# Optimization experiments

Measured on AMD Instinct MI355X. Metric: run time of the kernel, lower is better.

## Reference

```python
import jax, jax.numpy as jnp
import numpy as np

N_NODES = 50000
N_EDGES = 800000
IN_DIM = 128
EDGE_DIM = 16
HIDDEN = 128
N_LAYERS = 3
N_GRAPHS = 256
BN_EPS = 1e-5


def setup_inputs() -> dict:
    key = jax.random.key(0)
    ks = jax.random.split(key, 24)
    s = 0.05
    inp = {
        "x": jax.random.normal(ks[0], (N_NODES, IN_DIM), jnp.float32),
        "edge_index": jax.random.randint(ks[1], (2, N_EDGES), 0, N_NODES, jnp.int32),
        "edge_attr": jax.random.normal(ks[2], (N_EDGES, EDGE_DIM), jnp.float32),
        "batch": jnp.sort(jax.random.randint(ks[3], (N_NODES,), 0, N_GRAPHS, jnp.int32)),
        "n_graphs": N_GRAPHS,
        # input projection
        "lin_in_w": jax.random.normal(ks[4], (IN_DIM, HIDDEN), jnp.float32) * s,
        "lin_in_b": jnp.zeros((HIDDEN,), jnp.float32),
        # per-layer message MLP (stacked over layers)
        "msg_w1": jax.random.normal(ks[5], (N_LAYERS, HIDDEN + EDGE_DIM, HIDDEN), jnp.float32) * s,
        "msg_b1": jnp.zeros((N_LAYERS, HIDDEN), jnp.float32),
        "msg_w2": jax.random.normal(ks[6], (N_LAYERS, HIDDEN, HIDDEN), jnp.float32) * s,
        "msg_b2": jnp.zeros((N_LAYERS, HIDDEN), jnp.float32),
        # BatchNorm (eval mode: running stats)
        "bn_gamma": jnp.ones((N_LAYERS, HIDDEN), jnp.float32),
        "bn_beta": jnp.zeros((N_LAYERS, HIDDEN), jnp.float32),
        "bn_mean": jax.random.normal(ks[7], (N_LAYERS, HIDDEN), jnp.float32) * 0.01,
        "bn_var": jax.random.uniform(ks[8], (N_LAYERS, HIDDEN), jnp.float32, 0.5, 1.5),
        # GRUCell params (PyTorch layout: [3*H, H], gate order r,z,n)
        "gru_wih": jax.random.normal(ks[9], (N_LAYERS, 3 * HIDDEN, HIDDEN), jnp.float32) * s,
        "gru_whh": jax.random.normal(ks[10], (N_LAYERS, 3 * HIDDEN, HIDDEN), jnp.float32) * s,
        "gru_bih": jnp.zeros((N_LAYERS, 3 * HIDDEN), jnp.float32),
        "gru_bhh": jnp.zeros((N_LAYERS, 3 * HIDDEN), jnp.float32),
        # readout linear: [2H -> H]
        "ro_w": jax.random.normal(ks[11], (2 * HIDDEN, HIDDEN), jnp.float32) * s,
        "ro_b": jnp.zeros((HIDDEN,), jnp.float32),
    }
    return inp


def _gru_cell(x, h, wih, whh, bih, bhh):
    gi = x @ wih.T + bih  # [N, 3H]
    gh = h @ whh.T + bhh
    ir, iz, inn = jnp.split(gi, 3, axis=1)
    hr, hz, hn = jnp.split(gh, 3, axis=1)
    r = jax.nn.sigmoid(ir + hr)
    z = jax.nn.sigmoid(iz + hz)
    n = jnp.tanh(inn + r * hn)
    return (1.0 - z) * n + z * h


def reference(x, edge_index, edge_attr, batch, n_graphs,
              lin_in_w, lin_in_b, msg_w1, msg_b1, msg_w2, msg_b2,
              bn_gamma, bn_beta, bn_mean, bn_var,
              gru_wih, gru_whh, gru_bih, gru_bhh, ro_w, ro_b):
    h = jax.nn.relu(x @ lin_in_w + lin_in_b)  # [N, H]
    src, dst = edge_index[0], edge_index[1]
    n_nodes = h.shape[0]
    for l in range(N_LAYERS):
        m_in = jnp.concatenate([h[src], edge_attr], axis=1)  # [E, H+Ed]
        m = jax.nn.relu(m_in @ msg_w1[l] + msg_b1[l]) @ msg_w2[l] + msg_b2[l]  # [E, H]
        agg = jax.ops.segment_sum(m, dst, num_segments=n_nodes)  # scatter-add
        h_new = _gru_cell(agg, h, gru_wih[l], gru_whh[l], gru_bih[l], gru_bhh[l])
        bn = (h_new - bn_mean[l]) * jax.lax.rsqrt(bn_var[l] + BN_EPS) * bn_gamma[l] + bn_beta[l]
        h = h + bn  # dropout is identity in eval mode
    # readout: segment mean + segment max over graphs
    cnt = jax.ops.segment_sum(jnp.ones((n_nodes, 1), h.dtype), batch, num_segments=n_graphs)
    z_sum = jax.ops.segment_sum(h, batch, num_segments=n_graphs)
    z_mean = z_sum / jnp.maximum(cnt, 1.0)
    z_max = jax.ops.segment_max(h, batch, num_segments=n_graphs)
    z_max = jnp.where(cnt > 0, z_max, 0.0)  # empty graphs -> 0 (as in torch code)
    z = jax.nn.relu(jnp.concatenate([z_mean, z_max], axis=1) @ ro_w + ro_b)
    return z
```

## Files before the change

### kernel.cpp

```cpp
#include <hip/hip_runtime.h>
#include <math.h>

constexpr int NN = 50000;
constexpr int NE = 800000;
constexpr int H  = 128;
constexpr int ED = 16;
constexpr int NL = 3;
constexpr int NG = 256;
constexpr int NBINS = 50176;
constexpr int TE = 128;

typedef __attribute__((ext_vector_type(8))) short bf8;
typedef __attribute__((ext_vector_type(4))) float f32x4;

__device__ __forceinline__ unsigned short f2bf(float f) {
    unsigned u = __float_as_uint(f);
    unsigned r = (u + 0x7FFFu + ((u >> 16) & 1u)) >> 16;
    return (unsigned short)r;
}
__device__ __forceinline__ float bf2f(unsigned short b) {
    return __uint_as_float(((unsigned)b) << 16);
}
__device__ __forceinline__ float fsig(float x) {
    float e = __expf(fminf(-x, 80.f));
    return 1.f / (1.f + e);
}
__device__ __forceinline__ float ftanh_(float x) {
    float e = __expf(fminf(-2.f * x, 80.f));
    return (1.f - e) / (1.f + e);
}

__global__ __launch_bounds__(256) void k_sort_zero(int* __restrict__ counts) {
    int i = blockIdx.x * 256 + threadIdx.x;
    counts[i] = 0;
}

__global__ __launch_bounds__(256) void k_hist(const int* __restrict__ ei,
                                              int* __restrict__ counts) {
    int e = blockIdx.x * 256 + threadIdx.x;
    if (e < NE) atomicAdd(&counts[ei[NE + e]], 1);
}

__global__ __launch_bounds__(256) void k_scan1(const int* __restrict__ counts,
                                               int* __restrict__ incl,
                                               int* __restrict__ bsum) {
    __shared__ int s[256];
    int t = threadIdx.x;
    int i = blockIdx.x * 256 + t;
    int v = counts[i];
    s[t] = v;
    __syncthreads();
    #pragma unroll
    for (int off = 1; off < 256; off <<= 1) {
        int x = (t >= off) ? s[t - off] : 0;
        __syncthreads();
        s[t] += x;
        __syncthreads();
    }
    incl[i] = s[t];
    if (t == 255) bsum[blockIdx.x] = s[255];
}

__global__ __launch_bounds__(256) void k_scan2(int* __restrict__ bsum) {
    __shared__ int s[256];
    int t = threadIdx.x;
    int v = (t < 196) ? bsum[t] : 0;
    s[t] = v;
    __syncthreads();
    #pragma unroll
    for (int off = 1; off < 256; off <<= 1) {
        int x = (t >= off) ? s[t - off] : 0;
        __syncthreads();
        s[t] += x;
        __syncthreads();
    }
    if (t < 196) bsum[t] = s[t] - v;
}

__global__ __launch_bounds__(256) void k_scan3(const int* __restrict__ counts,
                                               const int* __restrict__ incl,
                                               const int* __restrict__ bsum,
                                               int* __restrict__ cur) {
    int i = blockIdx.x * 256 + threadIdx.x;
    cur[i] = incl[i] - counts[i] + bsum[blockIdx.x];
}

__global__ __launch_bounds__(256) void k_scatter_perm(const int* __restrict__ ei,
                                                      int* __restrict__ cur,
                                                      int* __restrict__ perm) {
    int e = blockIdx.x * 256 + threadIdx.x;
    if (e < NE) {
        int d = ei[NE + e];
        int pos = atomicAdd(&cur[d], 1);
        perm[pos] = e;
    }
}

__global__ __launch_bounds__(256) void k_gather(const int* __restrict__ ei,
                                                const float* __restrict__ ea,
                                                int* __restrict__ perm,
                                                int* __restrict__ dsts,
                                                unsigned short* __restrict__ ea_bf) {
    int i = blockIdx.x * 256 + threadIdx.x;
    if (i >= NE) return;
    int e = perm[i];
    perm[i] = ei[e];
    dsts[i] = ei[NE + e];
    const float4* sp = (const float4*)(ea + (size_t)e * ED);
    float4 v0 = sp[0], v1 = sp[1], v2 = sp[2], v3 = sp[3];
    union { uint4 u[2]; unsigned short sh[16]; } pk;
    pk.sh[0] = f2bf(v0.x); pk.sh[1] = f2bf(v0.y); pk.sh[2] = f2bf(v0.z); pk.sh[3] = f2bf(v0.w);
    pk.sh[4] = f2bf(v1.x); pk.sh[5] = f2bf(v1.y); pk.sh[6] = f2bf(v1.z); pk.sh[7] = f2bf(v1.w);
    pk.sh[8] = f2bf(v2.x); pk.sh[9] = f2bf(v2.y); pk.sh[10] = f2bf(v2.z); pk.sh[11] = f2bf(v2.w);
    pk.sh[12] = f2bf(v3.x); pk.sh[13] = f2bf(v3.y); pk.sh[14] = f2bf(v3.z); pk.sh[15] = f2bf(v3.w);
    uint4* d4 = (uint4*)(ea_bf + (size_t)i * 16);
    d4[0] = pk.u[0];
    d4[1] = pk.u[1];
}

__global__ __launch_bounds__(256) void k_prep(const float* __restrict__ wih,
                                              const float* __restrict__ whh,
                                              const float* __restrict__ w1,
                                              const float* __restrict__ w2,
                                              const float* __restrict__ lin_w,
                                              unsigned short* __restrict__ wgru,
                                              unsigned short* __restrict__ w1et,
                                              unsigned short* __restrict__ w2t,
                                              unsigned short* __restrict__ w1ht,
                                              unsigned short* __restrict__ winT) {
    int i = blockIdx.x * 256 + threadIdx.x;
    if (i < 294912) {
        int m = i / 147456, rem = i % 147456;
        wgru[i] = f2bf((m == 0 ? wih : whh)[rem]);
        return;
    }
    i -= 294912;
    if (i < NL * 128 * 32) {
        int l = i / 4096, rem = i % 4096;
        int n = rem >> 5, k = rem & 31;
        float v = (k < ED) ? w1[(size_t)l * 144 * 128 + (size_t)(128 + k) * 128 + n] : 0.f;
        w1et[i] = f2bf(v);
        return;
    }
    i -= NL * 128 * 32;
    if (i < NL * 128 * 128) {
        int l = i / 16384, rem = i % 16384;
        int n = rem >> 7, k = rem & 127;
        w2t[i] = f2bf(w2[(size_t)l * 16384 + (size_t)k * 128 + n]);
        return;
    }
    i -= NL * 128 * 128;
    if (i < NL * 128 * 128) {
        int l = i / 16384, rem = i % 16384;
        int n = rem >> 7, k = rem & 127;
        w1ht[i] = f2bf(w1[(size_t)l * 144 * 128 + (size_t)k * 128 + n]);
        return;
    }
    i -= NL * 128 * 128;
    if (i < 128 * 128) {
        int n = i >> 7, k = i & 127;
        winT[i] = f2bf(lin_w[k * 128 + n]);
    }
}

__global__ __launch_bounds__(256) void k_inproj(const float* __restrict__ x,
                                                const unsigned short* __restrict__ winT,
                                                const float* __restrict__ bias,
                                                const unsigned short* __restrict__ w1h0,
                                                float* __restrict__ h,
                                                unsigned short* __restrict__ p_bf,
                                                float* __restrict__ agg) {
    __shared__ unsigned short As[32][136];
    const int t = threadIdx.x;
    const int w = t >> 6, lane = t & 63, l15 = lane & 15, q = lane >> 4;
    const int n0 = blockIdx.x * 32;

    bf8 bfr[2][4];
    #pragma unroll
    for (int nt = 0; nt < 2; ++nt) {
        int n = w * 32 + nt * 16 + l15;
        #pragma unroll
        for (int ks = 0; ks < 4; ++ks)
            bfr[nt][ks] = *(const bf8*)(winT + (size_t)n * 128 + ks * 32 + q * 8);
    }

    {
        int r = t >> 3, cs = (t & 7) * 16;
        int row = n0 + r;
        float4 v[4];
        if (row < NN) {
            const float4* src = (const float4*)(x + (size_t)row * H + cs);
            #pragma unroll
            for (int j = 0; j < 4; ++j) v[j] = src[j];
        } else {
            #pragma unroll
            for (int j = 0; j < 4; ++j) v[j] = make_float4(0.f, 0.f, 0.f, 0.f);
        }
        union { uint4 u[2]; unsigned short s[16]; } pk;
        #pragma unroll
        for (int j = 0; j < 4; ++j) {
            pk.s[j * 4 + 0] = f2bf(v[j].x); pk.s[j * 4 + 1] = f2bf(v[j].y);
            pk.s[j * 4 + 2] = f2bf(v[j].z); pk.s[j * 4 + 3] = f2bf(v[j].w);
        }
        *(uint4*)&As[r][cs] = pk.u[0];
        *(uint4*)&As[r][cs + 8] = pk.u[1];
    }
    __syncthreads();

    {
        int r = t >> 3, cs = (t & 7) * 16;
        int row = n0 + r;
        if (row < NN) {
            float4 z = make_float4(0.f, 0.f, 0.f, 0.f);
            float4* dz = (float4*)(agg + (size_t)row * H + cs);
            dz[0] = z; dz[1] = z; dz[2] = z; dz[3] = z;
        }
    }

    f32x4 acc[2][2];
    #pragma unroll
    for (int mt = 0; mt < 2; ++mt)
        #pragma unroll
        for (int nt = 0; nt < 2; ++nt) acc[mt][nt] = {0.f, 0.f, 0.f, 0.f};

    #pragma unroll
    for (int ks = 0; ks < 4; ++ks) {
        #pragma unroll
        for (int mt = 0; mt < 2; ++mt) {
            bf8 af = *(const bf8*)&As[mt * 16 + l15][ks * 32 + q * 8];
            acc[mt][0] = __builtin_amdgcn_mfma_f32_16x16x32_bf16(af, bfr[0][ks], acc[mt][0], 0, 0, 0);
            acc[mt][1] = __builtin_amdgcn_mfma_f32_16x16x32_bf16(af, bfr[1][ks], acc[mt][1], 0, 0, 0);
        }
    }
    __syncthreads();

    #pragma unroll
    for (int nt = 0; nt < 2; ++nt) {
        int col = w * 32 + nt * 16 + l15;
        float bv = bias[col];
        #pragma unroll
        for (int mt = 0; mt < 2; ++mt) {
            #pragma unroll
            for (int r = 0; r < 4; ++r) {
                int nl = mt * 16 + q * 4 + r;
                int node = n0 + nl;
                float v = fmaxf(acc[mt][nt][r] + bv, 0.f);
                if (node < NN) h[(size_t)node * H + col] = v;
                As[nl][col] = f2bf(v);
            }
        }
    }
    __syncthreads();

    bf8 pfr[2][4];
    #pragma unroll
    for (int nt = 0; nt < 2; ++nt) {
        int n = w * 32 + nt * 16 + l15;
        #pragma unroll
        for (int ks = 0; ks < 4; ++ks)
            pfr[nt][ks] = *(const bf8*)(w1h0 + (size_t)n * 128 + ks * 32 + q * 8);
    }
    f32x4 accp[2][2];
    #pragma unroll
    for (int mt = 0; mt < 2; ++mt)
        #pragma unroll
        for (int nt = 0; nt < 2; ++nt) accp[mt][nt] = {0.f, 0.f, 0.f, 0.f};
    #pragma unroll
    for (int ks = 0; ks < 4; ++ks) {
        #pragma unroll
        for (int mt = 0; mt < 2; ++mt) {
            bf8 af = *(const bf8*)&As[mt * 16 + l15][ks * 32 + q * 8];
            accp[mt][0] = __builtin_amdgcn_mfma_f32_16x16x32_bf16(af, pfr[0][ks], accp[mt][0], 0, 0, 0);
            accp[mt][1] = __builtin_amdgcn_mfma_f32_16x16x32_bf16(af, pfr[1][ks], accp[mt][1], 0, 0, 0);
        }
    }
    #pragma unroll
    for (int nt = 0; nt < 2; ++nt) {
        int col = w * 32 + nt * 16 + l15;
        #pragma unroll
        for (int mt = 0; mt < 2; ++mt) {
            #pragma unroll
            for (int r = 0; r < 4; ++r) {
                int node = n0 + mt * 16 + q * 4 + r;
                if (node < NN) p_bf[(size_t)node * H + col] = f2bf(accp[mt][nt][r]);
            }
        }
    }
}

__global__ __launch_bounds__(256, 4) void k_edge_mfma(
        const unsigned short* __restrict__ p,
        const int* __restrict__ srcs,
        const int* __restrict__ dsts,
        const unsigned short* __restrict__ ea_bf,
        const unsigned short* __restrict__ w1et,
        const float* __restrict__ b1,
        const unsigned short* __restrict__ w2t,
        const float* __restrict__ b2,
        float* __restrict__ agg) {
    __shared__ unsigned short u_s[TE][136];
    __shared__ int src_s[TE], dst_s[TE];

    const int t    = threadIdx.x;
    const int w    = t >> 6;
    const int lane = t & 63;
    const int l15  = lane & 15;
    const int q    = lane >> 4;

    bf8 w1f[2];
    bf8 w2f[2][4];
    float b1v[2], b2v[2];
    #pragma unroll
    for (int nt = 0; nt < 2; ++nt) {
        int n = w * 32 + nt * 16 + l15;
        w1f[nt] = *(const bf8*)(w1et + (size_t)n * 32 + q * 8);
        #pragma unroll
        for (int ks = 0; ks < 4; ++ks)
            w2f[nt][ks] = *(const bf8*)(w2t + (size_t)n * 128 + ks * 32 + q * 8);
        b1v[nt] = b1[n];
        b2v[nt] = b2[n];
    }

    const f32x4 zero = {0.f, 0.f, 0.f, 0.f};

    for (int base = blockIdx.x * TE; base < NE; base += gridDim.x * TE) {
        if (t < TE) src_s[t] = srcs[base + t];
        else        dst_s[t - TE] = dsts[base + t - TE];
        __syncthreads();

        {
            int row = t >> 4, seg = t & 15;
            #pragma unroll
            for (int it = 0; it < 8; ++it) {
                int rr = row + 16 * it;
                *(uint4*)&u_s[rr][seg * 8] =
                    *(const uint4*)(p + (size_t)src_s[rr] * H + seg * 8);
            }
        }

        #pragma unroll
        for (int half = 0; half < 2; ++half) {
            f32x4 acc1[4][2];
            #pragma unroll
            for (int m4 = 0; m4 < 4; ++m4) {
                int mt = half * 4 + m4;
                bf8 af = {0, 0, 0, 0, 0, 0, 0, 0};
                if (q < 2)
                    af = *(const bf8*)(ea_bf + (size_t)(base + mt * 16 + l15) * 16 + q * 8);
                acc1[m4][0] = __builtin_amdgcn_mfma_f32_16x16x32_bf16(af, w1f[0], zero, 0, 0, 0);
                acc1[m4][1] = __builtin_amdgcn_mfma_f32_16x16x32_bf16(af, w1f[1], zero, 0, 0, 0);
            }
            if (half == 0) __syncthreads();
            #pragma unroll
            for (int m4 = 0; m4 < 4; ++m4) {
                #pragma unroll
                for (int r = 0; r < 4; ++r) {
                    int er = (half * 4 + m4) * 16 + q * 4 + r;
                    #pragma unroll
                    for (int nt = 0; nt < 2; ++nt) {
                        int col = w * 32 + nt * 16 + l15;
                        float v = acc1[m4][nt][r] + bf2f(u_s[er][col]) + b1v[nt];
                        u_s[er][col] = f2bf(fmaxf(v, 0.f));
                    }
                }
            }
        }
        __syncthreads();

        #pragma unroll
        for (int half = 0; half < 2; ++half) {
            f32x4 acc2[4][2];
            #pragma unroll
            for (int m4 = 0; m4 < 4; ++m4)
                #pragma unroll
                for (int nt = 0; nt < 2; ++nt) acc2[m4][nt] = zero;
            #pragma unroll
            for (int ks = 0; ks < 4; ++ks) {
                #pragma unroll
                for (int m4 = 0; m4 < 4; ++m4) {
                    int mt = half * 4 + m4;
                    bf8 af = *(const bf8*)&u_s[mt * 16 + l15][ks * 32 + q * 8];
                    acc2[m4][0] = __builtin_amdgcn_mfma_f32_16x16x32_bf16(af, w2f[0][ks], acc2[m4][0], 0, 0, 0);
                    acc2[m4][1] = __builtin_amdgcn_mfma_f32_16x16x32_bf16(af, w2f[1][ks], acc2[m4][1], 0, 0, 0);
                }
            }
            __syncthreads();
            #pragma unroll
            for (int m4 = 0; m4 < 4; ++m4) {
                #pragma unroll
                for (int r = 0; r < 4; ++r) {
                    int er = (half * 4 + m4) * 16 + q * 4 + r;
                    #pragma unroll
                    for (int nt = 0; nt < 2; ++nt) {
                        int col = w * 32 + nt * 16 + l15;
                        u_s[er][col] = f2bf(acc2[m4][nt][r] + b2v[nt]);
                    }
                }
            }
        }
        __syncthreads();

        {
            int c = t & 127, hh = t >> 7;
            float* aggc = agg + c;
            float sum = 0.f;
            int prev = dst_s[hh * 64];
            #pragma unroll 4
            for (int i = 0; i < 64; ++i) {
                int e = hh * 64 + i;
                int d = dst_s[e];
                float v = bf2f(u_s[e][c]);
                if (d != prev) {
                    atomicAdd(aggc + (size_t)prev * H, sum);
                    sum = 0.f;
                    prev = d;
                }
                sum += v;
            }
            atomicAdd(aggc + (size_t)prev * H, sum);
        }
        __syncthreads();
    }
}

__global__ __launch_bounds__(256) void k_gru_mfma(float* __restrict__ agg,
                                                  float* __restrict__ h,
                                                  const unsigned short* __restrict__ wih,
                                                  const unsigned short* __restrict__ whh,
                                                  const float* __restrict__ bih,
                                                  const float* __restrict__ bhh,
                                                  const float* __restrict__ gamma,
                                                  const float* __restrict__ beta,
                                                  const float* __restrict__ mean,
                                                  const float* __restrict__ var,
                                                  const unsigned short* __restrict__ w1h_next,
                                                  unsigned short* __restrict__ p_bf,
                                                  int* __restrict__ ro_z) {
    __shared__ unsigned short ab[32][136];
    __shared__ unsigned short hb[32][136];
    __shared__ float hf[32][132];
    const int t = threadIdx.x;
    const int w = t >> 6, lane = t & 63, l15 = lane & 15, q = lane >> 4;
    const int n0 = blockIdx.x * 32;

    {
        int r = t >> 3, cs = (t & 7) * 16;
        int row = n0 + r;
        float4 va[4], vh[4];
        if (row < NN) {
            const float4* sa = (const float4*)(agg + (size_t)row * H + cs);
            const float4* sh = (const float4*)(h + (size_t)row * H + cs);
            #pragma unroll
            for (int j = 0; j < 4; ++j) { va[j] = sa[j]; vh[j] = sh[j]; }
        } else {
            #pragma unroll
            for (int j = 0; j < 4; ++j) {
                va[j] = make_float4(0.f, 0.f, 0.f, 0.f);
                vh[j] = va[j];
            }
        }
        union { uint4 u[2]; unsigned short s[16]; } pa, ph;
        #pragma unroll
        for (int j = 0; j < 4; ++j) {
            pa.s[j * 4 + 0] = f2bf(va[j].x); pa.s[j * 4 + 1] = f2bf(va[j].y);
            pa.s[j * 4 + 2] = f2bf(va[j].z); pa.s[j * 4 + 3] = f2bf(va[j].w);
            ph.s[j * 4 + 0] = f2bf(vh[j].x); ph.s[j * 4 + 1] = f2bf(vh[j].y);
            ph.s[j * 4 + 2] = f2bf(vh[j].z); ph.s[j * 4 + 3] = f2bf(vh[j].w);
            *(float4*)&hf[r][cs + j * 4] = vh[j];
        }
        *(uint4*)&ab[r][cs] = pa.u[0];  *(uint4*)&ab[r][cs + 8] = pa.u[1];
        *(uint4*)&hb[r][cs] = ph.u[0];  *(uint4*)&hb[r][cs + 8] = ph.u[1];
    }
    __syncthreads();

    if (w1h_next != nullptr) {
        int r = t >> 3, cs = (t & 7) * 16;
        int row = n0 + r;
        if (row < NN) {
            float4 z = make_float4(0.f, 0.f, 0.f, 0.f);
            float4* dz = (float4*)(agg + (size_t)row * H + cs);
            dz[0] = z; dz[1] = z; dz[2] = z; dz[3] = z;
        }
    }
    if (ro_z != nullptr && blockIdx.x < 257) ro_z[blockIdx.x * 256 + t] = 0;

    f32x4 acc[2][2][3][2];
    #pragma unroll
    for (int mt = 0; mt < 2; ++mt)
        #pragma unroll
        for (int io = 0; io < 2; ++io)
            #pragma unroll
            for (int g = 0; g < 3; ++g)
                #pragma unroll
                for (int nt = 0; nt < 2; ++nt) acc[mt][io][g][nt] = {0.f, 0.f, 0.f, 0.f};

    #pragma unroll
    for (int ks = 0; ks < 4; ++ks) {
        bf8 a_a[2], a_h[2];
        #pragma unroll
        for (int mt = 0; mt < 2; ++mt) {
            a_a[mt] = *(const bf8*)&ab[mt * 16 + l15][ks * 32 + q * 8];
            a_h[mt] = *(const bf8*)&hb[mt * 16 + l15][ks * 32 + q * 8];
        }
        #pragma unroll
        for (int g = 0; g < 3; ++g) {
            #pragma unroll
            for (int nt = 0; nt < 2; ++nt) {
                int n = g * 128 + w * 32 + nt * 16 + l15;
                bf8 bi = *(const bf8*)(wih + (size_t)n * 128 + ks * 32 + q * 8);
                bf8 bh = *(const bf8*)(whh + (size_t)n * 128 + ks * 32 + q * 8);
                #pragma unroll
                for (int mt = 0; mt < 2; ++mt) {
                    acc[mt][0][g][nt] = __builtin_amdgcn_mfma_f32_16x16x32_bf16(a_a[mt], bi, acc[mt][0][g][nt], 0, 0, 0);
                    acc[mt][1][g][nt] = __builtin_amdgcn_mfma_f32_16x16x32_bf16(a_h[mt], bh, acc[mt][1][g][nt], 0, 0, 0);
                }
            }
        }
    }

    float rout[2][2][4];
    #pragma unroll
    for (int nt = 0; nt < 2; ++nt) {
        int col = w * 32 + nt * 16 + l15;
        float bir = bih[col], biz = bih[128 + col], bin = bih[256 + col];
        float bhr = bhh[col], bhz = bhh[128 + col], bhn = bhh[256 + col];
        float ga = gamma[col], be = beta[col], mu = mean[col];
        float iv = rsqrtf(var[col] + 1e-5f);
        #pragma unroll
        for (int mt = 0; mt < 2; ++mt) {
            #pragma unroll
            for (int r = 0; r < 4; ++r) {
                int nl = mt * 16 + q * 4 + r;
                int node = n0 + nl;
                float ir = acc[mt][0][0][nt][r] + bir;
                float iz = acc[mt][0][1][nt][r] + biz;
                float in = acc[mt][0][2][nt][r] + bin;
                float hr = acc[mt][1][0][nt][r] + bhr;
                float hz = acc[mt][1][1][nt][r] + bhz;
                float hn = acc[mt][1][2][nt][r] + bhn;
                float rg = fsig(ir + hr);
                float zg = fsig(iz + hz);
                float ng = ftanh_(in + rg * hn);
                float hv = hf[nl][col];
                float hnew = (1.f - zg) * ng + zg * hv;
                float bn = (hnew - mu) * iv * ga + be;
                float out = hv + bn;
                rout[nt][mt][r] = out;
                if (node < NN) h[(size_t)node * H + col] = out;
            }
        }
    }

    if (w1h_next != nullptr) {
        __syncthreads();
        #pragma unroll
        for (int nt = 0; nt < 2; ++nt) {
            int col = w * 32 + nt * 16 + l15;
            #pragma unroll
            for (int mt = 0; mt < 2; ++mt)
                #pragma unroll
                for (int r = 0; r < 4; ++r)
                    hb[mt * 16 + q * 4 + r][col] = f2bf(rout[nt][mt][r]);
        }
        __syncthreads();

        f32x4 accp[2][2];
        #pragma unroll
        for (int mt = 0; mt < 2; ++mt)
            #pragma unroll
            for (int nt = 0; nt < 2; ++nt) accp[mt][nt] = {0.f, 0.f, 0.f, 0.f};
        #pragma unroll
        for (int ks = 0; ks < 4; ++ks) {
            bf8 pf0, pf1;
            {
                int n = w * 32 + l15;
                pf0 = *(const bf8*)(w1h_next + (size_t)n * 128 + ks * 32 + q * 8);
                pf1 = *(const bf8*)(w1h_next + (size_t)(n + 16) * 128 + ks * 32 + q * 8);
            }
            #pragma unroll
            for (int mt = 0; mt < 2; ++mt) {
                bf8 af = *(const bf8*)&hb[mt * 16 + l15][ks * 32 + q * 8];
                accp[mt][0] = __builtin_amdgcn_mfma_f32_16x16x32_bf16(af, pf0, accp[mt][0], 0, 0, 0);
                accp[mt][1] = __builtin_amdgcn_mfma_f32_16x16x32_bf16(af, pf1, accp[mt][1], 0, 0, 0);
            }
        }
        #pragma unroll
        for (int nt = 0; nt < 2; ++nt) {
            int col = w * 32 + nt * 16 + l15;
            #pragma unroll
            for (int mt = 0; mt < 2; ++mt) {
                #pragma unroll
                for (int r = 0; r < 4; ++r) {
                    int node = n0 + mt * 16 + q * 4 + r;
                    if (node < NN) p_bf[(size_t)node * H + col] = f2bf(accp[mt][nt][r]);
                }
            }
        }
    }
}

__device__ __forceinline__ unsigned fkey(float f) {
    unsigned b = __float_as_uint(f);
    return (b & 0x80000000u) ? ~b : (b | 0x80000000u);
}
__device__ __forceinline__ float funkey(unsigned k) {
    unsigned b = (k & 0x80000000u) ? (k & 0x7FFFFFFFu) : ~k;
    return __uint_as_float(b);
}

__global__ __launch_bounds__(256) void k_ro_scan(const float* __restrict__ h,
                                                 const int* __restrict__ batch,
                                                 float* __restrict__ gsum,
                                                 unsigned* __restrict__ gmaxb,
                                                 float* __restrict__ gcnt) {
    __shared__ int bt_s[64];
    const int t = threadIdx.x;
    const int n0 = blockIdx.x * 64;
    if (t < 64) bt_s[t] = (n0 + t < NN) ? batch[n0 + t] : -1;
    __syncthreads();

    int c = t & 127, hh = t >> 7;
    float sum = 0.f, mx = -3.4e38f, cnt = 0.f;
    int prev = bt_s[hh * 32];
    #pragma unroll 4
    for (int i = 0; i < 32; ++i) {
        int e = hh * 32 + i;
        int g = bt_s[e];
        if (g != prev) {
            if (prev >= 0) {
                atomicAdd(&gsum[prev * H + c], sum);
                atomicMax(&gmaxb[prev * H + c], fkey(mx));
                if (c == 0) atomicAdd(&gcnt[prev], cnt);
            }
            sum = 0.f; mx = -3.4e38f; cnt = 0.f;
            prev = g;
        }
        if (g >= 0) {
            float v = h[(size_t)(n0 + e) * H + c];
            sum += v;
            mx = fmaxf(mx, v);
            cnt += 1.f;
        }
    }
    if (prev >= 0) {
        atomicAdd(&gsum[prev * H + c], sum);
        atomicMax(&gmaxb[prev * H + c], fkey(mx));
        if (c == 0) atomicAdd(&gcnt[prev], cnt);
    }
}

__global__ __launch_bounds__(128) void k_ro_final(const float* __restrict__ gsum,
                                                  const unsigned* __restrict__ gmaxb,
                                                  const float* __restrict__ gcnt,
                                                  const float* __restrict__ row,
                                                  const float* __restrict__ rob,
                                                  float* __restrict__ out) {
    __shared__ float cat[256];
    const int g = blockIdx.x, t = threadIdx.x;
    float cnt = gcnt[g];
    float inv = 1.f / fmaxf(cnt, 1.f);
    cat[t] = gsum[g * H + t] * inv;
    float mx = funkey(gmaxb[g * H + t]);
    cat[128 + t] = (cnt > 0.f) ? mx : 0.f;
    __syncthreads();
    float acc = rob[t];
    #pragma unroll 4
    for (int k = 0; k < 256; ++k) acc += cat[k] * row[k * H + t];
    out[g * H + t] = fmaxf(acc, 0.f);
}

extern "C" void kernel_launch(void* const* d_in, const int* in_sizes, int n_in,
                              void* d_out, int out_size, void* d_ws, size_t ws_size,
                              hipStream_t stream) {
    const float* x        = (const float*)d_in[0];
    const int*   ei       = (const int*)d_in[1];
    const float* ea       = (const float*)d_in[2];
    const int*   batch    = (const int*)d_in[3];
    const float* lin_in_w = (const float*)d_in[5];
    const float* lin_in_b = (const float*)d_in[6];
    const float* msg_w1   = (const float*)d_in[7];
    const float* msg_b1   = (const float*)d_in[8];
    const float* msg_w2   = (const float*)d_in[9];
    const float* msg_b2   = (const float*)d_in[10];
    const float* bn_gamma = (const float*)d_in[11];
    const float* bn_beta  = (const float*)d_in[12];
    const float* bn_mean  = (const float*)d_in[13];
    const float* bn_var   = (const float*)d_in[14];
    const float* gru_wih  = (const float*)d_in[15];
    const float* gru_whh  = (const float*)d_in[16];
    const float* gru_bih  = (const float*)d_in[17];
    const float* gru_bhh  = (const float*)d_in[18];
    const float* ro_w     = (const float*)d_in[19];
    const float* ro_b     = (const float*)d_in[20];

    float* ws = (float*)d_ws;
    float*          h     = ws;
    float*          agg   = ws + 6400000;
    unsigned short* p_bf  = (unsigned short*)(ws + 12800000);
    float*          gsum  = ws + 16000000;
    unsigned*       gmaxb = (unsigned*)(ws + 16032768);
    float*          gcnt  = ws + 16065536;
    unsigned short* wgru  = (unsigned short*)(ws + 16065792);
    unsigned short* w1et  = (unsigned short*)(ws + 16213248);
    unsigned short* w2t   = (unsigned short*)(ws + 16219392);
    unsigned short* w1ht  = (unsigned short*)(ws + 16243968);
    unsigned short* winT  = (unsigned short*)(ws + 16268544);
    int*            cnts  = (int*)(ws + 16276736);
    int*            incl  = (int*)(ws + 16326912);
    int*            cur   = (int*)(ws + 16377088);
    int*            bsum  = (int*)(ws + 16427264);
    int*            srcs  = (int*)(ws + 16427520);
    int*            dsts  = (int*)(ws + 17227520);
    unsigned short* ea_bf = (unsigned short*)(ws + 18027520);

    k_prep<<<1648, 256, 0, stream>>>(gru_wih, gru_whh, msg_w1, msg_w2, lin_in_w,
                                     wgru, w1et, w2t, w1ht, winT);
    k_sort_zero<<<196, 256, 0, stream>>>(cnts);
    k_hist<<<3125, 256, 0, stream>>>(ei, cnts);
    k_scan1<<<196, 256, 0, stream>>>(cnts, incl, bsum);
    k_scan2<<<1, 256, 0, stream>>>(bsum);
    k_scan3<<<196, 256, 0, stream>>>(cnts, incl, bsum, cur);
    k_scatter_perm<<<3125, 256, 0, stream>>>(ei, cur, srcs);
    k_gather<<<3125, 256, 0, stream>>>(ei, ea, srcs, dsts, ea_bf);

    k_inproj<<<1563, 256, 0, stream>>>(x, winT, lin_in_b, w1ht, h, p_bf, agg);

    for (int l = 0; l < NL; ++l) {
        k_edge_mfma<<<1024, 256, 0, stream>>>(p_bf, srcs, dsts, ea_bf,
                                              w1et + (size_t)l * 4096, msg_b1 + l * 128,
                                              w2t + (size_t)l * 16384, msg_b2 + l * 128,
                                              agg);
        const unsigned short* w1h_next = (l + 1 < NL) ? (w1ht + (size_t)(l + 1) * 16384) : nullptr;
        int* ro_z = (l == NL - 1) ? (int*)gsum : nullptr;
        k_gru_mfma<<<1563, 256, 0, stream>>>(agg, h,
                                             wgru + (size_t)l * 49152,
                                             wgru + (size_t)(NL + l) * 49152,
                                             gru_bih + l * 384, gru_bhh + l * 384,
                                             bn_gamma + l * 128, bn_beta + l * 128,
                                             bn_mean + l * 128, bn_var + l * 128,
                                             w1h_next, p_bf, ro_z);
    }

    k_ro_scan<<<782, 256, 0, stream>>>(h, batch, gsum, gmaxb, gcnt);
    k_ro_final<<<NG, 128, 0, stream>>>(gsum, gmaxb, gcnt, ro_w, ro_b, (float*)d_out);
}
```

Before: 803.3 us.

## Merge preprocessing kernels, single-block scan, prefetch edge indices, pair scatter-add channels

Folds the count-zeroing into the weight prep kernel and replaces the three-kernel prefix scan with a single 1024-thread block, cutting several small launches. In the edge kernel, src/dst indices for the next tile are double-buffered in shared memory so one barrier per iteration can be dropped. The segmented scatter-add now has each thread handle two adjacent channels over 32 edges instead of one channel over 64. The single-block scan serializes work onto one CU, and correctness of the removed trailing barrier depends on the next iteration's barrier ordering.

```diff
diff --git a/kernel.cpp b/kernel.cpp
--- a/kernel.cpp
+++ b/kernel.cpp
@@ -9,6 +9,7 @@
 constexpr int NG = 256;
 constexpr int NBINS = 50176;
 constexpr int TE = 128;
+constexpr int PREP_TOTAL = 294912 + NL*128*32 + NL*128*128 + NL*128*128 + 128*128;
 
 typedef __attribute__((ext_vector_type(8))) short bf8;
 typedef __attribute__((ext_vector_type(4))) float f32x4;
@@ -30,9 +31,53 @@
     return (1.f - e) / (1.f + e);
 }
 
-__global__ __launch_bounds__(256) void k_sort_zero(int* __restrict__ counts) {
+__global__ __launch_bounds__(256) void k_prep(const float* __restrict__ wih,
+                                              const float* __restrict__ whh,
+                                              const float* __restrict__ w1,
+                                              const float* __restrict__ w2,
+                                              const float* __restrict__ lin_w,
+                                              unsigned short* __restrict__ wgru,
+                                              unsigned short* __restrict__ w1et,
+                                              unsigned short* __restrict__ w2t,
+                                              unsigned short* __restrict__ w1ht,
+                                              unsigned short* __restrict__ winT,
+                                              int* __restrict__ cnts) {
     int i = blockIdx.x * 256 + threadIdx.x;
-    counts[i] = 0;
+    if (i < 294912) {
+        int m = i / 147456, rem = i % 147456;
+        wgru[i] = f2bf((m == 0 ? wih : whh)[rem]);
+        return;
+    }
+    i -= 294912;
+    if (i < NL * 128 * 32) {
+        int l = i / 4096, rem = i % 4096;
+        int n = rem >> 5, k = rem & 31;
+        float v = (k < ED) ? w1[(size_t)l * 144 * 128 + (size_t)(128 + k) * 128 + n] : 0.f;
+        w1et[i] = f2bf(v);
+        return;
+    }
+    i -= NL * 128 * 32;
+    if (i < NL * 128 * 128) {
+        int l = i / 16384, rem = i % 16384;
+        int n = rem >> 7, k = rem & 127;
+        w2t[i] = f2bf(w2[(size_t)l * 16384 + (size_t)k * 128 + n]);
+        return;
+    }
+    i -= NL * 128 * 128;
+    if (i < NL * 128 * 128) {
+        int l = i / 16384, rem = i % 16384;
+        int n = rem >> 7, k = rem & 127;
+        w1ht[i] = f2bf(w1[(size_t)l * 144 * 128 + (size_t)k * 128 + n]);
+        return;
+    }
+    i -= NL * 128 * 128;
+    if (i < 128 * 128) {
+        int n = i >> 7, k = i & 127;
+        winT[i] = f2bf(lin_w[k * 128 + n]);
+        return;
+    }
+    i -= 128 * 128;
+    if (i < NBINS) cnts[i] = 0;
 }
 
 __global__ __launch_bounds__(256) void k_hist(const int* __restrict__ ei,
@@ -41,48 +86,30 @@
     if (e < NE) atomicAdd(&counts[ei[NE + e]], 1);
 }
 
-__global__ __launch_bounds__(256) void k_scan1(const int* __restrict__ counts,
-                                               int* __restrict__ incl,
-                                               int* __restrict__ bsum) {
-    __shared__ int s[256];
-    int t = threadIdx.x;
-    int i = blockIdx.x * 256 + t;
-    int v = counts[i];
-    s[t] = v;
+__global__ __launch_bounds__(1024) void k_scan_all(const int* __restrict__ cnts,
+                                                   int* __restrict__ cur) {
+    __shared__ int s[1024];
+    const int t = threadIdx.x;
+    const int b0 = t * 49;
+    int sum = 0;
+    #pragma unroll 7
+    for (int i = 0; i < 49; ++i) sum += cnts[b0 + i];
+    s[t] = sum;
     __syncthreads();
     #pragma unroll
-    for (int off = 1; off < 256; off <<= 1) {
+    for (int off = 1; off < 1024; off <<= 1) {
         int x = (t >= off) ? s[t - off] : 0;
         __syncthreads();
         s[t] += x;
         __syncthreads();
     }
-    incl[i] = s[t];
-    if (t == 255) bsum[blockIdx.x] = s[255];
-}
-
-__global__ __launch_bounds__(256) void k_scan2(int* __restrict__ bsum) {
-    __shared__ int s[256];
-    int t = threadIdx.x;
-    int v = (t < 196) ? bsum[t] : 0;
-    s[t] = v;
-    __syncthreads();
-    #pragma unroll
-    for (int off = 1; off < 256; off <<= 1) {
-        int x = (t >= off) ? s[t - off] : 0;
-        __syncthreads();
-        s[t] += x;
-        __syncthreads();
-    }
-    if (t < 196) bsum[t] = s[t] - v;
-}
-
-__global__ __launch_bounds__(256) void k_scan3(const int* __restrict__ counts,
-                                               const int* __restrict__ incl,
-                                               const int* __restrict__ bsum,
-                                               int* __restrict__ cur) {
-    int i = blockIdx.x * 256 + threadIdx.x;
-    cur[i] = incl[i] - counts[i] + bsum[blockIdx.x];
+    int run = s[t] - sum;
+    #pragma unroll 7
+    for (int i = 0; i < 49; ++i) {
+        int c = cnts[b0 + i];
+        cur[b0 + i] = run;
+        run += c;
+    }
 }
 
 __global__ __launch_bounds__(256) void k_scatter_perm(const int* __restrict__ ei,
@@ -118,51 +145,6 @@
     d4[1] = pk.u[1];
 }
 
-__global__ __launch_bounds__(256) void k_prep(const float* __restrict__ wih,
-                                              const float* __restrict__ whh,
-                                              const float* __restrict__ w1,
-                                              const float* __restrict__ w2,
-                                              const float* __restrict__ lin_w,
-                                              unsigned short* __restrict__ wgru,
-                                              unsigned short* __restrict__ w1et,
-                                              unsigned short* __restrict__ w2t,
-                                              unsigned short* __restrict__ w1ht,
-                                              unsigned short* __restrict__ winT) {
-    int i = blockIdx.x * 256 + threadIdx.x;
-    if (i < 294912) {
-        int m = i / 147456, rem = i % 147456;
-        wgru[i] = f2bf((m == 0 ? wih : whh)[rem]);
-        return;
-    }
-    i -= 294912;
-    if (i < NL * 128 * 32) {
-        int l = i / 4096, rem = i % 4096;
-        int n = rem >> 5, k = rem & 31;
-        float v = (k < ED) ? w1[(size_t)l * 144 * 128 + (size_t)(128 + k) * 128 + n] : 0.f;
-        w1et[i] = f2bf(v);
-        return;
-    }
-    i -= NL * 128 * 32;
-    if (i < NL * 128 * 128) {
-        int l = i / 16384, rem = i % 16384;
-        int n = rem >> 7, k = rem & 127;
-        w2t[i] = f2bf(w2[(size_t)l * 16384 + (size_t)k * 128 + n]);
-        return;
-    }
-    i -= NL * 128 * 128;
-    if (i < NL * 128 * 128) {
-        int l = i / 16384, rem = i % 16384;
-        int n = rem >> 7, k = rem & 127;
-        w1ht[i] = f2bf(w1[(size_t)l * 144 * 128 + (size_t)k * 128 + n]);
-        return;
-    }
-    i -= NL * 128 * 128;
-    if (i < 128 * 128) {
-        int n = i >> 7, k = i & 127;
-        winT[i] = f2bf(lin_w[k * 128 + n]);
-    }
-}
-
 __global__ __launch_bounds__(256) void k_inproj(const float* __restrict__ x,
                                                 const unsigned short* __restrict__ winT,
                                                 const float* __restrict__ bias,
@@ -299,7 +281,7 @@
         const float* __restrict__ b2,
         float* __restrict__ agg) {
     __shared__ unsigned short u_s[TE][136];
-    __shared__ int src_s[TE], dst_s[TE];
+    __shared__ int src_s[2][TE], dst_s[2][TE];
 
     const int t    = threadIdx.x;
     const int w    = t >> 6;
@@ -323,9 +305,16 @@
 
     const f32x4 zero = {0.f, 0.f, 0.f, 0.f};
 
+    {
+        int base0 = blockIdx.x * TE;
+        if (base0 < NE) {
+            if (t < TE) src_s[0][t] = srcs[base0 + t];
+            else        dst_s[0][t - TE] = dsts[base0 + t - TE];
+        }
+    }
+    int pb = 0;
+
     for (int base = blockIdx.x * TE; base < NE; base += gridDim.x * TE) {
-        if (t < TE) src_s[t] = srcs[base + t];
-        else        dst_s[t - TE] = dsts[base + t - TE];
         __syncthreads();
 
         {
@@ -334,7 +323,7 @@
             for (int it = 0; it < 8; ++it) {
                 int rr = row + 16 * it;
                 *(uint4*)&u_s[rr][seg * 8] =
-                    *(const uint4*)(p + (size_t)src_s[rr] * H + seg * 8);
+                    *(const uint4*)(p + (size_t)src_s[pb][rr] * H + seg * 8);
             }
         }
 
@@ -401,25 +390,37 @@
         __syncthreads();
 
         {
-            int c = t & 127, hh = t >> 7;
-            float* aggc = agg + c;
-            float sum = 0.f;
-            int prev = dst_s[hh * 64];
+            int nbase = base + gridDim.x * TE;
+            if (nbase < NE) {
+                if (t < TE) src_s[1 - pb][t] = srcs[nbase + t];
+                else        dst_s[1 - pb][t - TE] = dsts[nbase + t - TE];
+            }
+        }
+
+        {
+            int q4 = t >> 6;
+            int cp = t & 63;
+            float* aggc = agg + (cp << 1);
+            float s0 = 0.f, s1 = 0.f;
+            int prev = dst_s[pb][q4 * 32];
             #pragma unroll 4
-            for (int i = 0; i < 64; ++i) {
-                int e = hh * 64 + i;
-                int d = dst_s[e];
-                float v = bf2f(u_s[e][c]);
+            for (int i = 0; i < 32; ++i) {
+                int e = q4 * 32 + i;
+                int d = dst_s[pb][e];
+                unsigned v = *(const unsigned*)&u_s[e][cp << 1];
                 if (d != prev) {
-                    atomicAdd(aggc + (size_t)prev * H, sum);
-                    sum = 0.f;
+                    atomicAdd(aggc + (size_t)prev * H, s0);
+                    atomicAdd(aggc + (size_t)prev * H + 1, s1);
+                    s0 = 0.f; s1 = 0.f;
                     prev = d;
                 }
-                sum += v;
-            }
-            atomicAdd(aggc + (size_t)prev * H, sum);
-        }
-        __syncthreads();
+                s0 += bf2f((unsigned short)(v & 0xFFFFu));
+                s1 += bf2f((unsigned short)(v >> 16));
+            }
+            atomicAdd(aggc + (size_t)prev * H, s0);
+            atomicAdd(aggc + (size_t)prev * H + 1, s1);
+        }
+        pb ^= 1;
     }
 }
 
@@ -706,20 +707,15 @@
     unsigned short* w1ht  = (unsigned short*)(ws + 16243968);
     unsigned short* winT  = (unsigned short*)(ws + 16268544);
     int*            cnts  = (int*)(ws + 16276736);
-    int*            incl  = (int*)(ws + 16326912);
-    int*            cur   = (int*)(ws + 16377088);
-    int*            bsum  = (int*)(ws + 16427264);
-    int*            srcs  = (int*)(ws + 16427520);
-    int*            dsts  = (int*)(ws + 17227520);
-    unsigned short* ea_bf = (unsigned short*)(ws + 18027520);
-
-    k_prep<<<1648, 256, 0, stream>>>(gru_wih, gru_whh, msg_w1, msg_w2, lin_in_w,
-                                     wgru, w1et, w2t, w1ht, winT);
-    k_sort_zero<<<196, 256, 0, stream>>>(cnts);
+    int*            cur   = (int*)(ws + 16326912);
+    int*            srcs  = (int*)(ws + 16377088);
+    int*            dsts  = (int*)(ws + 17177088);
+    unsigned short* ea_bf = (unsigned short*)(ws + 17977088);
+
+    k_prep<<<1844, 256, 0, stream>>>(gru_wih, gru_whh, msg_w1, msg_w2, lin_in_w,
+                                     wgru, w1et, w2t, w1ht, winT, cnts);
     k_hist<<<3125, 256, 0, stream>>>(ei, cnts);
-    k_scan1<<<196, 256, 0, stream>>>(cnts, incl, bsum);
-    k_scan2<<<1, 256, 0, stream>>>(bsum);
-    k_scan3<<<196, 256, 0, stream>>>(cnts, incl, bsum, cur);
+    k_scan_all<<<1, 1024, 0, stream>>>(cnts, cur);
     k_scatter_perm<<<3125, 256, 0, stream>>>(ei, cur, srcs);
     k_gather<<<3125, 256, 0, stream>>>(ei, ea, srcs, dsts, ea_bf);
 
```

Result: slower. 859.3 us (+7.0%).
